# Kernel optimization log

Hardware: AMD Instinct MI355X
Metric: run time of the kernel (lower is better)

Reference implementation:

```python
import jax, jax.numpy as jnp
import numpy as np

N_QUBITS = 6
Q_DEPTH = 2
K = 3
PAD = 1
EPS = 1e-9
Q_DIM = 2 ** N_QUBITS


def _rx(t):
    c = jnp.cos(t / 2).astype(jnp.complex64)
    s = jnp.sin(t / 2).astype(jnp.complex64)
    return jnp.stack([jnp.stack([c, -1j * s]), jnp.stack([-1j * s, c])])


def _ry(t):
    c = jnp.cos(t / 2).astype(jnp.complex64)
    s = jnp.sin(t / 2).astype(jnp.complex64)
    return jnp.stack([jnp.stack([c, -s]), jnp.stack([s, c])])


def _u3(t, p, lm):
    c = jnp.cos(t / 2).astype(jnp.complex64)
    s = jnp.sin(t / 2).astype(jnp.complex64)
    ep = jnp.exp(1j * p.astype(jnp.complex64))
    el = jnp.exp(1j * lm.astype(jnp.complex64))
    return jnp.stack([jnp.stack([c, -el * s]), jnp.stack([ep * s, ep * el * c])])


def _apply_1q(st, U, wire):
    # st: (bsz, 2**n) complex; wire 0 = most significant bit (torchquantum layout)
    s = st.reshape(-1, 2 ** wire, 2, 2 ** (N_QUBITS - wire - 1))
    s = jnp.einsum('ab,nxby->nxay', U, s)
    return s.reshape(-1, Q_DIM)


def _apply_cnot(st, wire):
    # CNOT with control=wire, target=wire+1 (adjacent)
    s = st.reshape(-1, 2 ** wire, 2, 2, 2 ** (N_QUBITS - wire - 2))
    s = jnp.stack([s[:, :, 0], s[:, :, 1, ::-1]], axis=2)
    return s.reshape(-1, Q_DIM)


def _quantum_forward(x, inp_scale, in_proj_w, in_proj_b, weights, meas_w, out_proj_w, out_proj_b):
    B, C, H, W = x.shape
    # Unfold(kernel=3, pad=1, stride=1) -> (B, C*9, H*W), channel-major then (kh, kw)
    xp = jnp.pad(x, ((0, 0), (0, 0), (PAD, PAD), (PAD, PAD)))
    pat = jnp.stack([xp[:, :, i:i + H, j:j + W] for i in range(K) for j in range(K)], axis=2)
    pat = pat.reshape(B, C * K * K, H * W).transpose(0, 2, 1).reshape(-1, C * K * K)
    pf = pat * inp_scale
    xq = pf @ in_proj_w.T + in_proj_b                       # (bsz, 64)
    xq = xq / (jnp.linalg.norm(xq, axis=-1, keepdims=True) + EPS)
    st = xq.astype(jnp.complex64)                           # (bsz, 2**n)
    for l in range(Q_DEPTH):
        for i in range(N_QUBITS):
            st = _apply_1q(st, _rx(weights[l, i, 0]), i)
            st = _apply_1q(st, _ry(weights[l, i, 1]), i)
        for i in range(N_QUBITS - 1):
            st = _apply_cnot(st, i)
        for i in range(N_QUBITS):
            st = _apply_1q(st, _ry(weights[l, i, 2]), i)
    for i in range(N_QUBITS):
        st = _apply_1q(st, _u3(meas_w[i, 0], meas_w[i, 1], meas_w[i, 2]), i)
    probs = st.real ** 2 + st.imag ** 2                     # |amp|^2
    out = probs @ out_proj_w.T + out_proj_b                 # (bsz, out_channels)
    return out.reshape(B, H * W, -1).transpose(0, 2, 1).reshape(B, -1, H, W)


def setup_inputs() -> dict:
    key = jax.random.key(0)
    ks = jax.random.split(key, 8)
    C_IN, C_OUT = 32, 64
    patch_dim = C_IN * K * K  # 288
    x = jax.random.normal(ks[0], (16, C_IN, 64, 64), dtype=jnp.float32)
    inp_scale = jnp.ones((patch_dim,), dtype=jnp.float32)
    in_proj_w = jax.random.normal(ks[1], (Q_DIM, patch_dim), dtype=jnp.float32) / np.sqrt(patch_dim)
    in_proj_b = jax.random.normal(ks[2], (Q_DIM,), dtype=jnp.float32) / np.sqrt(patch_dim)
    weights = 0.1 * jax.random.normal(ks[3], (Q_DEPTH, N_QUBITS, 3), dtype=jnp.float32)
    meas_w = 0.1 * jax.random.normal(ks[4], (N_QUBITS, 3), dtype=jnp.float32)
    out_proj_w = jax.random.normal(ks[5], (C_OUT, Q_DIM), dtype=jnp.float32) / np.sqrt(Q_DIM)
    out_proj_b = jax.random.normal(ks[6], (C_OUT,), dtype=jnp.float32) / np.sqrt(Q_DIM)
    return {"x": x, "inp_scale": inp_scale, "in_proj_w": in_proj_w, "in_proj_b": in_proj_b,
            "weights": weights, "meas_w": meas_w, "out_proj_w": out_proj_w, "out_proj_b": out_proj_b}


def reference(x, inp_scale, in_proj_w, in_proj_b, weights, meas_w, out_proj_w, out_proj_b):
    return _quantum_forward(x, inp_scale, in_proj_w, in_proj_b, weights, meas_w, out_proj_w, out_proj_b)
```

## Files before the change

### kernel.cpp

```cpp
#include <hip/hip_runtime.h>

typedef float f32x4 __attribute__((ext_vector_type(4)));
typedef short bf16x8 __attribute__((ext_vector_type(8)));

#define NB   16
#define CIN  32
#define HW   64
#define CKK  288
#define QD   64

#define WS_WSF 0
#define WS_MCF 18432
#define WS_WOF 26624

__device__ __forceinline__ unsigned short f2bf(float f) {
  unsigned u = __builtin_bit_cast(unsigned, f);
  u += 0x7FFFu + ((u >> 16) & 1u);
  return (unsigned short)(u >> 16);
}

struct C2 { float r, i; };
struct M2 { C2 a, b, c, d; };

__device__ __forceinline__ C2 cmul(C2 x, C2 y) { return { x.r*y.r - x.i*y.i, x.r*y.i + x.i*y.r }; }
__device__ __forceinline__ C2 cadd(C2 x, C2 y) { return { x.r + y.r, x.i + y.i }; }
__device__ __forceinline__ M2 mmul(M2 X, M2 Y) {
  return { cadd(cmul(X.a, Y.a), cmul(X.b, Y.c)),
           cadd(cmul(X.a, Y.b), cmul(X.b, Y.d)),
           cadd(cmul(X.c, Y.a), cmul(X.d, Y.c)),
           cadd(cmul(X.c, Y.b), cmul(X.d, Y.d)) };
}

__device__ __forceinline__ M2 mRX(float t) {
  float s, c; __sincosf(t * 0.5f, &s, &c);
  return { {c,0.f}, {0.f,-s}, {0.f,-s}, {c,0.f} };
}
__device__ __forceinline__ M2 mRY(float t) {
  float s, c; __sincosf(t * 0.5f, &s, &c);
  return { {c,0.f}, {-s,0.f}, {s,0.f}, {c,0.f} };
}
__device__ __forceinline__ M2 mU3(float t, float p, float lm) {
  float s, c; __sincosf(t * 0.5f, &s, &c);
  float sp, cp; __sincosf(p, &sp, &cp);
  float sl, cl; __sincosf(lm, &sl, &cl);
  float spl, cpl; __sincosf(p + lm, &spl, &cpl);
  return { {c,0.f}, {-cl*s, -sl*s}, {cp*s, sp*s}, {cpl*c, spl*c} };
}

__global__ __launch_bounds__(256) void prep_kernel(
    const float* __restrict__ in_proj_w, const float* __restrict__ inp_scale,
    const float* __restrict__ weights, const float* __restrict__ meas_w,
    const float* __restrict__ out_proj_w, unsigned short* __restrict__ ws)
{
  const int tid = threadIdx.x, blk = blockIdx.x;

  if (blk < 36) {
    int f = blk, kk = f >> 2, jt = f & 3;
#pragma unroll
    for (int u = 0; u < 2; ++u) {
      int r = tid * 2 + u;
      int lw = r >> 3, e = r & 7;
      int row = jt * 16 + (lw & 15);
      int ch = (lw >> 4) * 8 + e;
      int src = ch * 9 + kk;
      ws[WS_WSF + f * 512 + r] = f2bf(in_proj_w[row * CKK + src] * inp_scale[src]);
    }
    return;
  }
  if (blk == 36) {
#pragma unroll
    for (int m = 0; m < 16; ++m) {
      int d = tid * 16 + m;
      int f = d >> 9, r = d & 511;
      int lw = r >> 3, e = r & 7;
      int kk = f >> 2, ot = f & 3;
      int src = (ot * 16 + (lw & 15)) * 64 + kk * 32 + (lw >> 4) * 8 + e;
      ws[WS_WOF + d] = f2bf(out_proj_w[src]);
    }
    return;
  }

  const int lane = tid & 63, wid = tid >> 6;
  const int col = (blk - 37) * 4 + wid;

  float re, im;
  {
    C2 amp = {1.f, 0.f};
#pragma unroll
    for (int q = 0; q < 6; ++q) {
      M2 G = mmul(mRY(weights[q * 3 + 1]), mRX(weights[q * 3 + 0]));
      int rb = (lane >> (5 - q)) & 1;
      int cb = (col >> (5 - q)) & 1;
      C2 sel = rb ? (cb ? G.d : G.c) : (cb ? G.b : G.a);
      amp = cmul(amp, sel);
    }
    re = amp.r; im = amp.i;
  }

  const int t1 = (lane ^ (lane >> 1) ^ (lane >> 2) ^ (lane >> 3) ^ (lane >> 4) ^ (lane >> 5)) & 63;
  const int t2 = (lane ^ (lane >> 2) ^ (lane >> 4)) & 63;

  auto applyM = [&](int maskShuf, int rb, M2 U) {
    float arr = rb ? U.d.r : U.a.r, ari = rb ? U.d.i : U.a.i;
    float brr = rb ? U.c.r : U.b.r, bri = rb ? U.c.i : U.b.i;
    float pre = __shfl_xor(re, maskShuf);
    float pim = __shfl_xor(im, maskShuf);
    float nr = arr * re - ari * im + brr * pre - bri * pim;
    float ni = arr * im + ari * re + brr * pim + bri * pre;
    re = nr; im = ni;
  };

  const int MK1[6] = {0x01, 0x03, 0x06, 0x0C, 0x18, 0x30};
  const int MK2[6] = {0x01, 0x02, 0x05, 0x0A, 0x14, 0x28};

#pragma unroll
  for (int q = 0; q < 6; ++q) {
    const int b = 5 - q;
    M2 U = mmul(mmul(mRY(weights[18 + q * 3 + 1]), mRX(weights[18 + q * 3 + 0])),
                mRY(weights[q * 3 + 2]));
    applyM(MK1[b], (t1 >> b) & 1, U);
  }
#pragma unroll
  for (int q = 0; q < 6; ++q) {
    const int b = 5 - q;
    M2 U = mmul(mU3(meas_w[q * 3], meas_w[q * 3 + 1], meas_w[q * 3 + 2]),
                mRY(weights[18 + q * 3 + 2]));
    applyM(MK2[b], (t2 >> b) & 1, U);
  }

  unsigned short* McF = ws + WS_MCF;
  const int nRe = t2 >> 4, c16r = t2 & 15;
  const int kk = col >> 5, gc = (col >> 3) & 3, e = col & 7;
  const int off = (gc * 16 + c16r) * 8 + e;
  McF[(kk * 8 + nRe) * 512 + off]     = f2bf(re);
  McF[(kk * 8 + 4 + nRe) * 512 + off] = f2bf(im);
}

#define LDA 72
#define LDO 65

__global__ __launch_bounds__(256) void main_kernel(
    const float* __restrict__ x, const float* __restrict__ b_in,
    const float* __restrict__ b_out, const unsigned short* __restrict__ ws,
    float* __restrict__ out)
{
  __shared__ __align__(16) unsigned char smem[18432];
  unsigned short* a_lds = (unsigned short*)smem;
  unsigned short* p_lds = (unsigned short*)(smem + 9216);
  float* o_lds = (float*)smem;

  const int tid = threadIdx.x, lane = tid & 63, wid = tid >> 6;
  const int g = lane >> 4, c16 = lane & 15;
  const int blk = (blockIdx.x & 7) * 128 + (blockIdx.x >> 3);
  const int b = blk >> 6, h = blk & 63;

  const unsigned short* WsF = ws + WS_WSF;
  const unsigned short* McF = ws + WS_MCF;
  const unsigned short* WoF = ws + WS_WOF;

  f32x4 acc[4];
#pragma unroll
  for (int jt = 0; jt < 4; ++jt) { float bi = b_in[jt * 16 + c16]; acc[jt] = f32x4{bi, bi, bi, bi}; }

  const int ar = wid * 16 + c16;
  const float* xb = x + b * CIN * HW * HW;
  const int xw0 = (ar >= 1) ? ar - 1 : 0;
  const int xw2 = (ar <= 62) ? ar + 1 : 63;
  const bool ok0 = (ar >= 1), ok2 = (ar <= 62);

#pragma unroll
  for (int kk = 0; kk < 9; ++kk) {
    const int di = kk / 3, dj = kk % 3;
    const int y = h + di - 1;
    bf16x8 af;
    if ((unsigned)y < 64u) {
      const int xwc = (dj == 0) ? xw0 : (dj == 1) ? ar : xw2;
      const bool okx = (dj == 0) ? ok0 : (dj == 1) ? true : ok2;
      const float* py = xb + y * 64 + xwc;
#pragma unroll
      for (int i = 0; i < 8; ++i) {
        float v = py[(g * 8 + i) * 4096];
        v = okx ? v : 0.f;
        af[i] = (short)f2bf(v);
      }
    } else {
#pragma unroll
      for (int i = 0; i < 8; ++i) af[i] = 0;
    }
#pragma unroll
    for (int jt = 0; jt < 4; ++jt) {
      bf16x8 bf_ = *(const bf16x8*)(WsF + (kk * 4 + jt) * 512 + lane * 8);
      acc[jt] = __builtin_amdgcn_mfma_f32_16x16x32_bf16(af, bf_, acc[jt], 0, 0, 0);
    }
  }

  float s[4];
#pragma unroll
  for (int r = 0; r < 4; ++r) {
    float t = acc[0][r] * acc[0][r] + acc[1][r] * acc[1][r] +
              acc[2][r] * acc[2][r] + acc[3][r] * acc[3][r];
    t += __shfl_xor(t, 1); t += __shfl_xor(t, 2); t += __shfl_xor(t, 4); t += __shfl_xor(t, 8);
    s[r] = 1.f / (sqrtf(t) + 1e-9f);
  }
#pragma unroll
  for (int jt = 0; jt < 4; ++jt)
#pragma unroll
    for (int r = 0; r < 4; ++r)
      a_lds[(wid * 16 + g * 4 + r) * LDA + jt * 16 + c16] = f2bf(acc[jt][r] * s[r]);

  f32x4 uv[8];
#pragma unroll
  for (int n = 0; n < 8; ++n) uv[n] = f32x4{0.f, 0.f, 0.f, 0.f};
#pragma unroll
  for (int kk = 0; kk < 2; ++kk) {
    bf16x8 af = *(const bf16x8*)(a_lds + (wid * 16 + c16) * LDA + kk * 32 + g * 8);
#pragma unroll
    for (int n = 0; n < 8; ++n) {
      bf16x8 bf_ = *(const bf16x8*)(McF + (kk * 8 + n) * 512 + lane * 8);
      uv[n] = __builtin_amdgcn_mfma_f32_16x16x32_bf16(af, bf_, uv[n], 0, 0, 0);
    }
  }

#pragma unroll
  for (int n = 0; n < 4; ++n)
#pragma unroll
    for (int r = 0; r < 4; ++r) {
      float p = uv[n][r] * uv[n][r] + uv[n + 4][r] * uv[n + 4][r];
      p_lds[(wid * 16 + g * 4 + r) * LDA + n * 16 + c16] = f2bf(p);
    }

  f32x4 o[4];
#pragma unroll
  for (int ot = 0; ot < 4; ++ot) { float bo = b_out[ot * 16 + c16]; o[ot] = f32x4{bo, bo, bo, bo}; }
#pragma unroll
  for (int kk = 0; kk < 2; ++kk) {
    bf16x8 af = *(const bf16x8*)(p_lds + (wid * 16 + c16) * LDA + kk * 32 + g * 8);
#pragma unroll
    for (int ot = 0; ot < 4; ++ot) {
      bf16x8 bf_ = *(const bf16x8*)(WoF + (kk * 4 + ot) * 512 + lane * 8);
      o[ot] = __builtin_amdgcn_mfma_f32_16x16x32_bf16(af, bf_, o[ot], 0, 0, 0);
    }
  }

  __syncthreads();
#pragma unroll
  for (int ot = 0; ot < 4; ++ot)
#pragma unroll
    for (int r = 0; r < 4; ++r)
      o_lds[(ot * 16 + c16) * LDO + wid * 16 + g * 4 + r] = o[ot][r];
  __syncthreads();

  float* outb = out + (size_t)b * QD * HW * HW + h * HW;
#pragma unroll
  for (int it = 0; it < 16; ++it) {
    int orow = it * 4 + wid;
    outb[orow * (HW * HW) + lane] = o_lds[orow * LDO + lane];
  }
}

extern "C" void kernel_launch(void* const* d_in, const int* in_sizes, int n_in,
                              void* d_out, int out_size, void* d_ws, size_t ws_size,
                              hipStream_t stream) {
  const float* x          = (const float*)d_in[0];
  const float* inp_scale  = (const float*)d_in[1];
  const float* in_proj_w  = (const float*)d_in[2];
  const float* in_proj_b  = (const float*)d_in[3];
  const float* weights    = (const float*)d_in[4];
  const float* meas_w     = (const float*)d_in[5];
  const float* out_proj_w = (const float*)d_in[6];
  const float* out_proj_b = (const float*)d_in[7];
  unsigned short* ws = (unsigned short*)d_ws;

  prep_kernel<<<53, 256, 0, stream>>>(in_proj_w, inp_scale, weights, meas_w, out_proj_w, ws);
  main_kernel<<<NB * HW, 256, 0, stream>>>(x, in_proj_b, out_proj_b, ws, (float*)d_out);
}
```

Before: 24.35 us.

## Pre-transpose input to channel-last bf16 in prep kernel for vector loads

The prep kernel gains 1024 extra blocks that convert x from NCHW fp32 into an NHWC bf16 copy in the workspace. The main kernel then fetches each patch row's 8 channels with one 16-byte load instead of eight strided fp32 loads and per-element conversions. In exchange, x is read once by prep and written again as half-size bf16, costing an extra pass and a larger prep launch.

After: 24.61 us. No clear change (+1.1%).

```diff
diff --git a/kernel.cpp b/kernel.cpp
--- a/kernel.cpp
+++ b/kernel.cpp
@@ -12,6 +12,7 @@
 #define WS_WSF 0
 #define WS_MCF 18432
 #define WS_WOF 26624
+#define WS_XQF 30720
 
 __device__ __forceinline__ unsigned short f2bf(float f) {
   unsigned u = __builtin_bit_cast(unsigned, f);
@@ -48,14 +49,28 @@
 }
 
 __global__ __launch_bounds__(256) void prep_kernel(
+    const float* __restrict__ x,
     const float* __restrict__ in_proj_w, const float* __restrict__ inp_scale,
     const float* __restrict__ weights, const float* __restrict__ meas_w,
     const float* __restrict__ out_proj_w, unsigned short* __restrict__ ws)
 {
   const int tid = threadIdx.x, blk = blockIdx.x;
 
-  if (blk < 36) {
-    int f = blk, kk = f >> 2, jt = f & 3;
+  if (blk < 1024) {
+    const int b = blk >> 6, y = blk & 63;
+    const int lane = tid & 63, w = tid >> 6;
+    const float* src = x + ((b * CIN + w * 8) * HW + y) * HW + lane;
+    unsigned short* dst = ws + WS_XQF + (size_t)((b * HW + y) * HW + lane) * CIN + w * 8;
+    bf16x8 o8;
+#pragma unroll
+    for (int j = 0; j < 8; ++j) o8[j] = (short)f2bf(src[j * HW * HW]);
+    *(bf16x8*)dst = o8;
+    return;
+  }
+  const int blk2 = blk - 1024;
+
+  if (blk2 < 36) {
+    int f = blk2, kk = f >> 2, jt = f & 3;
 #pragma unroll
     for (int u = 0; u < 2; ++u) {
       int r = tid * 2 + u;
@@ -67,7 +82,7 @@
     }
     return;
   }
-  if (blk == 36) {
+  if (blk2 == 36) {
 #pragma unroll
     for (int m = 0; m < 16; ++m) {
       int d = tid * 16 + m;
@@ -81,7 +96,7 @@
   }
 
   const int lane = tid & 63, wid = tid >> 6;
-  const int col = (blk - 37) * 4 + wid;
+  const int col = (blk2 - 37) * 4 + wid;
 
   float re, im;
   {
@@ -140,9 +155,8 @@
 #define LDO 65
 
 __global__ __launch_bounds__(256) void main_kernel(
-    const float* __restrict__ x, const float* __restrict__ b_in,
-    const float* __restrict__ b_out, const unsigned short* __restrict__ ws,
-    float* __restrict__ out)
+    const float* __restrict__ b_in, const float* __restrict__ b_out,
+    const unsigned short* __restrict__ ws, float* __restrict__ out)
 {
   __shared__ __align__(16) unsigned char smem[18432];
   unsigned short* a_lds = (unsigned short*)smem;
@@ -157,13 +171,13 @@
   const unsigned short* WsF = ws + WS_WSF;
   const unsigned short* McF = ws + WS_MCF;
   const unsigned short* WoF = ws + WS_WOF;
+  const unsigned short* xqb = ws + WS_XQF + (size_t)b * (HW * HW * CIN);
 
   f32x4 acc[4];
 #pragma unroll
   for (int jt = 0; jt < 4; ++jt) { float bi = b_in[jt * 16 + c16]; acc[jt] = f32x4{bi, bi, bi, bi}; }
 
   const int ar = wid * 16 + c16;
-  const float* xb = x + b * CIN * HW * HW;
   const int xw0 = (ar >= 1) ? ar - 1 : 0;
   const int xw2 = (ar <= 62) ? ar + 1 : 63;
   const bool ok0 = (ar >= 1), ok2 = (ar <= 62);
@@ -175,14 +189,11 @@
     bf16x8 af;
     if ((unsigned)y < 64u) {
       const int xwc = (dj == 0) ? xw0 : (dj == 1) ? ar : xw2;
+      af = *(const bf16x8*)(xqb + (y * 64 + xwc) * CIN + g * 8);
       const bool okx = (dj == 0) ? ok0 : (dj == 1) ? true : ok2;
-      const float* py = xb + y * 64 + xwc;
-#pragma unroll
-      for (int i = 0; i < 8; ++i) {
-        float v = py[(g * 8 + i) * 4096];
-        v = okx ? v : 0.f;
-        af[i] = (short)f2bf(v);
-      }
+      if (!okx)
+#pragma unroll
+        for (int i = 0; i < 8; ++i) af[i] = 0;
     } else {
 #pragma unroll
       for (int i = 0; i < 8; ++i) af[i] = 0;
@@ -271,6 +282,6 @@
   const float* out_proj_b = (const float*)d_in[7];
   unsigned short* ws = (unsigned short*)d_ws;
 
-  prep_kernel<<<53, 256, 0, stream>>>(in_proj_w, inp_scale, weights, meas_w, out_proj_w, ws);
-  main_kernel<<<NB * HW, 256, 0, stream>>>(x, in_proj_b, out_proj_b, ws, (float*)d_out);
-}
+  prep_kernel<<<1077, 256, 0, stream>>>(x, in_proj_w, inp_scale, weights, meas_w, out_proj_w, ws);
+  main_kernel<<<NB * HW, 256, 0, stream>>>(in_proj_b, out_proj_b, ws, (float*)d_out);
+}
```
